# Performance work log

Hardware: AMD Instinct MI355X
Metric: run time of the kernel (lower is better)

Reference implementation:

```python
import jax, jax.numpy as jnp
import numpy as np

N = 120000          # number of edges
DN = 256            # dim_node
DE = 256            # dim_edge
DA = 256            # dim_atten
H = 8               # num_heads
d_n = DN // H       # 32
d_e = DE // H       # 32
d_o = DA // H       # 32
SIGMA = 1.0
SCALE = 0.02


def setup_inputs() -> dict:
    key = jax.random.key(0)
    ks = jax.random.split(key, 16)
    rn = lambda k, s: jax.random.normal(k, s, dtype=jnp.float32)
    HID = DN + 2 * DE  # nn_edge hidden width (bidirectional variant) = 768
    return {
        "query": rn(ks[0], (N, DN)),
        "edge": rn(ks[1], (N, DE)),
        "value": rn(ks[2], (N, DN)),
        "reverse_edge": rn(ks[3], (N, DE)),
        "src_centers": rn(ks[4], (N, 3)),
        "dst_centers": rn(ks[5], (N, 3)),
        # nn_edge: Linear(2*DN+2*DE -> HID) + ReLU, Linear(HID -> DE)
        "We1": rn(ks[6], (2 * DN + 2 * DE, HID)) * SCALE,
        "be1": jnp.zeros((HID,), jnp.float32),
        "We2": rn(ks[7], (HID, DE)) * SCALE,
        "be2": jnp.zeros((DE,), jnp.float32),
        # proj_query / proj_edge / proj_value: single Linear layers
        "Wq": rn(ks[8], (DN, DN)) * SCALE,
        "bq": jnp.zeros((DN,), jnp.float32),
        "Wpe": rn(ks[9], (DE, DE)) * SCALE,
        "bpe": jnp.zeros((DE,), jnp.float32),
        "Wv": rn(ks[10], (DN, DA)) * SCALE,
        "bv": jnp.zeros((DA,), jnp.float32),
        # attention nn (MLP of 1x1 convs over channel dim): (d_n+d_e)->(d_n+d_e)->d_o
        "A1": rn(ks[11], (d_n + d_e, d_n + d_e)) * SCALE,
        "a1": jnp.zeros((d_n + d_e,), jnp.float32),
        "A2": rn(ks[12], (d_n + d_e, d_o)) * SCALE,
        "a2": jnp.zeros((d_o,), jnp.float32),
    }


def reference(query, edge, value, reverse_edge, src_centers, dst_centers,
              We1, be1, We2, be2, Wq, bq, Wpe, bpe, Wv, bv, A1, a1, A2, a2):
    # --- edge feature MLP (bidirectional) ---
    ef_in = jnp.concatenate([query, edge, reverse_edge, value], axis=1)  # [N, 1024]
    h = jax.nn.relu(ef_in @ We1 + be1)
    edge_feature = h @ We2 + be2                                         # [N, DE]

    # --- gaussian distance weights from object centers ---
    dist = jnp.linalg.norm(src_centers - dst_centers, axis=1, keepdims=True)  # [N, 1]
    dw = jnp.exp(-dist ** 2 / (2.0 * SIGMA ** 2))                             # [N, 1]
    edge_feature = edge_feature * dw

    # --- multi-head 'fat' attention ---
    value_proj = value @ Wv + bv                                  # [N, DA]
    q = (query @ Wq + bq).reshape(N, d_n, H)                      # [N, d_n, H]
    e = (edge @ Wpe + bpe).reshape(N, d_e, H)                     # [N, d_e, H]
    x_in = jnp.concatenate([q, e], axis=1)                        # [N, d_n+d_e, H]
    # MLP over channel dim (1x1 conv equivalents), ReLU on hidden only
    h2 = jax.nn.relu(jnp.einsum('nch,co->noh', x_in, A1) + a1[None, :, None])
    logits = jnp.einsum('nch,co->noh', h2, A2) + a2[None, :, None]  # [N, d_o, H]
    prob = jax.nn.softmax(logits, axis=1)

    # distance-reweighted attention, renormalized over channel dim
    combined = prob * dw[:, :, None]                               # [N, d_o, H]
    combined = combined / (combined.sum(axis=1, keepdims=True) + 1e-10)
    weights_avg = combined.mean(axis=2)                            # [N, d_o]
    # sum_d weights_avg[n,d] * value_proj[n,a]  ==  weights_avg.sum(1) * value_proj
    # (avoids materializing the [N, d_o, DA] broadcast the torch code creates)
    x = weights_avg.sum(axis=1, keepdims=True) * value_proj        # [N, DA]
    return (x, edge_feature, prob)
```

## Files before the change

### kernel.cpp

```cpp
#include <hip/hip_runtime.h>
#include <stdint.h>

typedef float  f32x4 __attribute__((ext_vector_type(4)));
typedef _Float16 f16x8 __attribute__((ext_vector_type(8)));
typedef _Float16 f16x4 __attribute__((ext_vector_type(4)));

#define OFF_We1T 0
#define OFF_We2T 786432
#define OFF_WqT  983040
#define OFF_WpeT 1048576
#define OFF_WvT  1114112
#define OFF_A1T  1179648
#define OFF_A2T  1183744
#define NHALF    1185792

__device__ __forceinline__ void gl_lds16(const void* g, void* l) {
  __builtin_amdgcn_global_load_lds((const __attribute__((address_space(1))) uint32_t*)g,
                                   (__attribute__((address_space(3))) uint32_t*)l, 16, 0, 0);
}

__device__ __forceinline__ int bake(int k, int n) {
  return (k & ~63) | ((((k >> 3) ^ n) & 7) << 3) | (k & 7);
}

__global__ __launch_bounds__(256) void prep_weights(
    const float* We1, const float* We2, const float* Wq, const float* Wpe,
    const float* Wv, const float* A1, const float* A2,
    const float* bq, const float* bpe,
    _Float16* wsh, float* bqp, float* bpep) {
  int i = blockIdx.x * 256 + threadIdx.x;
  if (i < OFF_We2T) {
    int n = i >> 10, k = i & 1023;
    wsh[i] = (_Float16)We1[bake(k, n) * 768 + n];
  } else if (i < OFF_WqT) {
    int j = i - OFF_We2T; int n = j / 768, k = j - n * 768;
    wsh[i] = (_Float16)We2[bake(k, n) * 256 + n];
  } else if (i < OFF_WpeT) {
    int j = i - OFF_WqT; int n = j >> 8, k = j & 255;
    int sc = ((n & 31) << 3) + (n >> 5);
    wsh[i] = (_Float16)Wq[bake(k, n) * 256 + sc];
  } else if (i < OFF_WvT) {
    int j = i - OFF_WpeT; int n = j >> 8, k = j & 255;
    int sc = ((n & 31) << 3) + (n >> 5);
    wsh[i] = (_Float16)Wpe[bake(k, n) * 256 + sc];
  } else if (i < OFF_A1T) {
    int j = i - OFF_WvT; int n = j >> 8, k = j & 255;
    wsh[i] = (_Float16)Wv[bake(k, n) * 256 + n];
  } else if (i < OFF_A2T) {
    int j = i - OFF_A1T; int o = j >> 6, c = j & 63;
    wsh[i] = (_Float16)A1[bake(c, o) * 64 + o];
  } else if (i < NHALF) {
    int j = i - OFF_A2T; int o = j >> 6, c = j & 63;
    wsh[i] = (_Float16)A2[bake(c, o) * 32 + o];
  } else if (i < NHALF + 256) {
    int j = i - NHALF;
    bqp[j] = bq[((j & 31) << 3) + (j >> 5)];
  } else if (i < NHALF + 512) {
    int j = i - NHALF - 256;
    bpep[j] = bpe[((j & 31) << 3) + (j >> 5)];
  }
}

__global__ __launch_bounds__(256) void prep_dw(const float* s, const float* d,
                                               float* dw, float* fw, int N) {
  int n = blockIdx.x * 256 + threadIdx.x;
  if (n >= N) return;
  float dx = s[3*n] - d[3*n], dy = s[3*n+1] - d[3*n+1], dz = s[3*n+2] - d[3*n+2];
  float d2 = dx*dx + dy*dy + dz*dz;
  float w = expf(-0.5f * d2);
  dw[n] = w;
  fw[n] = w / (w + 1e-10f);
}

struct GP {
  const float* q; const float* e; const float* v; const float* rev;
  const _Float16* wsh;
  const float* be1; const float* be2; const float* bv;
  const float* bqp; const float* bpep;
  const float* dw; const float* fw;
  float* outb;
  int N; int SPLIT;
};

template <int MODE>
__global__ __launch_bounds__(256) void gemm_k(GP p) {
  __shared__ __align__(16) _Float16 smh[4][8192];
  __shared__ float biasL[128];
  __shared__ float scaleL[128];
  const int t = threadIdx.x;
  const int w = t >> 6, lane = t & 63, lr = lane & 15, lk = lane >> 4;
  const int NBX = (MODE == 1) ? 2 : 6;
  const int flat = blockIdx.y * NBX + blockIdx.x;
  const int xcd = flat & 7, kk2 = flat >> 3;
  const int CH = gridDim.y >> 3;
  const int nb = kk2 % NBX;
  const int mb = xcd * CH + kk2 / NBX;
  const int N = p.N, SPLIT = p.SPLIT;
  const int MT = (N + 127) >> 7;
  if (mb >= MT) return;
  const int wrow = (w >> 1) * 64, wcol = (w & 1) * 64;
  float* Xf  = p.outb;
  float* EFf = p.outb + (size_t)N * 256;
  float* PRf = p.outb + (size_t)N * 512;
  _Float16* hp1 = (_Float16*)Xf;
  _Float16* hp2 = (_Float16*)PRf;

  int K, KT; size_t boff; int g = 0, nbl = nb;
  if (MODE == 0)      { K = 1024; KT = 16; boff = (size_t)nb * 128 * 1024; }
  else if (MODE == 1) { K = 768;  KT = 12; boff = OFF_We2T + (size_t)nb * 128 * 768; }
  else { K = 256; KT = 4; g = nb >> 1; nbl = nb & 1;
         size_t wb = (g == 0) ? (size_t)OFF_WqT : (g == 1) ? (size_t)OFF_WpeT : (size_t)OFF_WvT;
         boff = wb + (size_t)nbl * 128 * 256; }
  const _Float16* Bt = p.wsh + boff;

  if (t < 128) {
    int gr = mb * 128 + t; if (gr > N - 1) gr = N - 1;
    if (MODE == 0) biasL[t] = p.be1[nb * 128 + t];
    else if (MODE == 1) { biasL[t] = p.be2[nb * 128 + t]; scaleL[t] = p.dw[gr]; }
    else {
      if (g == 0)      biasL[t] = p.bqp[nbl * 128 + t];
      else if (g == 1) biasL[t] = p.bpep[nbl * 128 + t];
      else { biasL[t] = p.bv[nbl * 128 + t]; scaleL[t] = p.fw[gr]; }
    }
  }

  auto stageB = [&](int kt, int buf) {
#pragma unroll
    for (int i = 0; i < 4; ++i)
      gl_lds16(Bt + (size_t)(i * 32 + (t >> 3)) * K + kt * 64 + (t & 7) * 8,
               (char*)smh[2 + buf] + i * 4096 + w * 1024);
  };
  auto stageA_dma = [&](int kt, int buf) {
    const _Float16* hr = (mb * 128 < SPLIT)
        ? hp1 + (size_t)mb * 128 * 768
        : hp2 + (size_t)(mb * 128 - SPLIT) * 768;
    int rmax = N - 1 - mb * 128;
#pragma unroll
    for (int i = 0; i < 4; ++i) {
      int rl = i * 32 + (t >> 3); if (rl > rmax) rl = rmax;
      gl_lds16(hr + (size_t)rl * 768 + kt * 64 + (t & 7) * 8,
               (char*)smh[buf] + i * 4096 + w * 1024);
    }
  };
  auto loadA = [&](int kt, float4* pre) {
    const float* As; int cc0;
    if (MODE == 0) {
      int gg = kt >> 2;
      As = (gg == 0) ? p.q : (gg == 1) ? p.e : (gg == 2) ? p.rev : p.v;
      cc0 = (kt & 3) * 64;
    } else {
      As = (g == 0) ? p.q : (g == 1) ? p.e : p.v; cc0 = kt * 64;
    }
#pragma unroll
    for (int i = 0; i < 8; ++i) {
      int id = i * 256 + t, row = id >> 4, c4 = id & 15;
      int gr = mb * 128 + row; if (gr > N - 1) gr = N - 1;
      pre[i] = *(const float4*)(As + (size_t)gr * 256 + cc0 + c4 * 4);
    }
  };
  auto writeA = [&](const float4* pre, int buf) {
#pragma unroll
    for (int i = 0; i < 8; ++i) {
      int id = i * 256 + t, row = id >> 4, c4 = id & 15;
      f16x4 hv; hv.x = (_Float16)pre[i].x; hv.y = (_Float16)pre[i].y;
      hv.z = (_Float16)pre[i].z; hv.w = (_Float16)pre[i].w;
      int off = row * 64 + (((((c4 >> 1) ^ row) & 7) << 3) | ((c4 & 1) << 2));
      *(f16x4*)(&smh[buf][off]) = hv;
    }
  };

  f32x4 acc[4][4] = {};
  float4 pre[8];
  if (MODE == 1) stageA_dma(0, 0);
  stageB(0, 0);
  if (MODE != 1) { loadA(0, pre); writeA(pre, 0); }

  for (int kt = 0; kt < KT; ++kt) {
    const int cur = kt & 1;
    __syncthreads();
    const bool more = (kt + 1 < KT);
    if (more) {
      if (MODE == 1) stageA_dma(kt + 1, cur ^ 1);
      else loadA(kt + 1, pre);
      stageB(kt + 1, cur ^ 1);
    }
    const _Float16* Ab = smh[cur];
    const _Float16* Bb = smh[2 + cur];
#pragma unroll
    for (int ks = 0; ks < 2; ++ks) {
      f16x8 af[4], bf[4];
#pragma unroll
      for (int i = 0; i < 4; ++i)
        af[i] = *(const f16x8*)(Ab + (wrow + i * 16 + lr) * 64 + (((ks * 4 + lk) ^ (lr & 7)) << 3));
#pragma unroll
      for (int j = 0; j < 4; ++j)
        bf[j] = *(const f16x8*)(Bb + (wcol + j * 16 + lr) * 64 + (((ks * 4 + lk) ^ (lr & 7)) << 3));
#pragma unroll
      for (int i = 0; i < 4; ++i)
#pragma unroll
        for (int j = 0; j < 4; ++j)
          acc[i][j] = __builtin_amdgcn_mfma_f32_16x16x32_f16(af[i], bf[j], acc[i][j], 0, 0, 0);
    }
    if (more && MODE != 1) writeA(pre, cur ^ 1);
  }
  __syncthreads();

  const bool f16out = (MODE == 0) || (MODE == 2 && g < 2);
  if (f16out) {
    _Float16* Cl = (_Float16*)smh;
#pragma unroll
    for (int i = 0; i < 4; ++i)
#pragma unroll
      for (int j = 0; j < 4; ++j)
#pragma unroll
        for (int ii = 0; ii < 4; ++ii) {
          int r = wrow + i * 16 + lk * 4 + ii, c = wcol + j * 16 + lr;
          float val = acc[i][j][ii] + biasL[c];
          if (MODE == 0) val = fmaxf(val, 0.f);
          Cl[r * 136 + c] = (_Float16)val;
        }
    __syncthreads();
#pragma unroll
    for (int i = 0; i < 8; ++i) {
      int id = i * 256 + t, row = id >> 4, ch = id & 15;
      int gr = mb * 128 + row;
      if (gr < N) {
        f16x8 val = *(const f16x8*)(Cl + row * 136 + ch * 8);
        if (MODE == 0) {
          _Float16* hrow = (gr < SPLIT) ? hp1 + (size_t)gr * 768
                                        : hp2 + (size_t)(gr - SPLIT) * 768;
          int b64 = nb * 128 + ((ch >> 3) << 6);
          *(f16x8*)(hrow + b64 + (((ch ^ gr) & 7) << 3)) = val;
        } else {
          int j0 = nbl * 128 + ch * 8;
          int q = j0 >> 5;
          int G = ((j0 >> 3) & 3) | ((g == 1) ? 4 : 0);
          *(f16x8*)(hp2 + ((size_t)gr * 8 + q) * 64 + (((G ^ q) & 7) << 3)) = val;
        }
      }
    }
  } else {
    float* Cf = (float*)smh;
#pragma unroll
    for (int pp = 0; pp < 2; ++pp) {
      __syncthreads();
      if ((w >> 1) == pp) {
#pragma unroll
        for (int i = 0; i < 4; ++i)
#pragma unroll
          for (int j = 0; j < 4; ++j)
#pragma unroll
            for (int ii = 0; ii < 4; ++ii) {
              int rl = i * 16 + lk * 4 + ii, c = wcol + j * 16 + lr;
              Cf[rl * 132 + c] = (acc[i][j][ii] + biasL[c]) * scaleL[pp * 64 + rl];
            }
      }
      __syncthreads();
#pragma unroll
      for (int i = 0; i < 8; ++i) {
        int id = i * 256 + t, row = id >> 5, ch = id & 31;
        int gr = mb * 128 + pp * 64 + row;
        if (gr < N) {
          float4 val = *(const float4*)(Cf + row * 132 + ch * 4);
          float* dst = (MODE == 1) ? EFf + (size_t)gr * 256 + nb * 128 + ch * 4
                                   : Xf  + (size_t)gr * 256 + nbl * 128 + ch * 4;
          *(float4*)dst = val;
        }
      }
    }
  }
}

__global__ __launch_bounds__(256) void attn_k(GP p, const float* a1, const float* a2) {
  __shared__ __align__(16) char sm[28928];
  _Float16* xinl = (_Float16*)sm;
  _Float16* A1l  = (_Float16*)(sm + 8192);
  _Float16* A2l  = (_Float16*)(sm + 16384);
  float*    lg   = (float*)(sm + 20480);
  const int t = threadIdx.x;
  const int w = t >> 6, lane = t & 63, lr = lane & 15, lk = lane >> 4;
  const int N = p.N;
  float* PRf = p.outb + (size_t)N * 512;
  const _Float16* xing = (const _Float16*)PRf;
  size_t rowbase = (size_t)blockIdx.x * 64;

#pragma unroll
  for (int i = 0; i < 2; ++i)
    gl_lds16(xing + (rowbase + i * 32 + (t >> 3)) * 64 + (t & 7) * 8,
             sm + i * 4096 + w * 1024);
#pragma unroll
  for (int i = 0; i < 2; ++i)
    gl_lds16(p.wsh + OFF_A1T + (size_t)(i * 32 + (t >> 3)) * 64 + (t & 7) * 8,
             sm + 8192 + i * 4096 + w * 1024);
  gl_lds16(p.wsh + OFF_A2T + (size_t)(t >> 3) * 64 + (t & 7) * 8,
           sm + 16384 + w * 1024);
  __syncthreads();

  f32x4 acc1[4] = {};
#pragma unroll
  for (int ks = 0; ks < 2; ++ks) {
    f16x8 a = *(const f16x8*)(xinl + (w * 16 + lr) * 64 + (((ks * 4 + lk) ^ (lr & 7)) << 3));
#pragma unroll
    for (int j = 0; j < 4; ++j) {
      f16x8 b = *(const f16x8*)(A1l + (j * 16 + lr) * 64 + (((ks * 4 + lk) ^ (lr & 7)) << 3));
      acc1[j] = __builtin_amdgcn_mfma_f32_16x16x32_f16(a, b, acc1[j], 0, 0, 0);
    }
  }
  __syncthreads();
#pragma unroll
  for (int j = 0; j < 4; ++j) {
    float bb = a1[j * 16 + lr];
#pragma unroll
    for (int ii = 0; ii < 4; ++ii) {
      float hv = fmaxf(acc1[j][ii] + bb, 0.f);
      int row2 = w * 16 + lk * 4 + ii, col = j * 16 + lr;
      xinl[row2 * 64 + (((((col >> 3) ^ row2) & 7) << 3) | (col & 7))] = (_Float16)hv;
    }
  }
  __syncthreads();
  f32x4 acc2[2] = {};
#pragma unroll
  for (int ks = 0; ks < 2; ++ks) {
    f16x8 a = *(const f16x8*)(xinl + (w * 16 + lr) * 64 + (((ks * 4 + lk) ^ (lr & 7)) << 3));
#pragma unroll
    for (int j = 0; j < 2; ++j) {
      f16x8 b = *(const f16x8*)(A2l + (j * 16 + lr) * 64 + (((ks * 4 + lk) ^ (lr & 7)) << 3));
      acc2[j] = __builtin_amdgcn_mfma_f32_16x16x32_f16(a, b, acc2[j], 0, 0, 0);
    }
  }
#pragma unroll
  for (int j = 0; j < 2; ++j) {
    float bb = a2[j * 16 + lr];
#pragma unroll
    for (int ii = 0; ii < 4; ++ii)
      lg[(w * 16 + lk * 4 + ii) * 33 + j * 16 + lr] = acc2[j][ii] + bb;
  }
  __syncthreads();
  {
    int r = t >> 2, pq = t & 3;
    float vv[8];
#pragma unroll
    for (int jj = 0; jj < 8; ++jj) vv[jj] = lg[r * 33 + pq * 8 + jj];
    float mx = vv[0];
#pragma unroll
    for (int jj = 1; jj < 8; ++jj) mx = fmaxf(mx, vv[jj]);
    mx = fmaxf(mx, __shfl_xor(mx, 1));
    mx = fmaxf(mx, __shfl_xor(mx, 2));
    float s = 0.f;
#pragma unroll
    for (int jj = 0; jj < 8; ++jj) { vv[jj] = __expf(vv[jj] - mx); s += vv[jj]; }
    s += __shfl_xor(s, 1);
    s += __shfl_xor(s, 2);
    float inv = 1.f / s;
#pragma unroll
    for (int jj = 0; jj < 8; ++jj) lg[r * 33 + pq * 8 + jj] = vv[jj] * inv;
  }
  __syncthreads();
#pragma unroll
  for (int i = 0; i < 8; ++i) {
    int id = i * 256 + t; int hh = id & 7, o = (id >> 3) & 31, nl = id >> 8;
    PRf[(rowbase / 8 + nl) * 256 + o * 8 + hh] = lg[(nl * 8 + hh) * 33 + o];
  }
}

extern "C" void kernel_launch(void* const* d_in, const int* in_sizes, int n_in,
                              void* d_out, int out_size, void* d_ws, size_t ws_size,
                              hipStream_t stream) {
  const float* query = (const float*)d_in[0];
  const float* edge  = (const float*)d_in[1];
  const float* value = (const float*)d_in[2];
  const float* rev   = (const float*)d_in[3];
  const float* srcc  = (const float*)d_in[4];
  const float* dstc  = (const float*)d_in[5];
  const float* We1 = (const float*)d_in[6];  const float* be1 = (const float*)d_in[7];
  const float* We2 = (const float*)d_in[8];  const float* be2 = (const float*)d_in[9];
  const float* Wq  = (const float*)d_in[10]; const float* bq  = (const float*)d_in[11];
  const float* Wpe = (const float*)d_in[12]; const float* bpe = (const float*)d_in[13];
  const float* Wv  = (const float*)d_in[14]; const float* bv  = (const float*)d_in[15];
  const float* A1  = (const float*)d_in[16]; const float* a1  = (const float*)d_in[17];
  const float* A2  = (const float*)d_in[18]; const float* a2  = (const float*)d_in[19];
  const int N = in_sizes[0] / 256;

  _Float16* wsh = (_Float16*)d_ws;
  float* wsf = (float*)d_ws;
  float* dwA  = wsf + NHALF / 2;
  float* fwA  = dwA + N;
  float* bqp  = fwA + N;
  float* bpep = bqp + 256;

  prep_weights<<<(NHALF + 512 + 255) / 256, 256, 0, stream>>>(
      We1, We2, Wq, Wpe, Wv, A1, A2, bq, bpe, wsh, bqp, bpep);
  prep_dw<<<(N + 255) / 256, 256, 0, stream>>>(srcc, dstc, dwA, fwA, N);

  GP p;
  p.q = query; p.e = edge; p.v = value; p.rev = rev;
  p.wsh = wsh; p.be1 = be1; p.be2 = be2; p.bv = bv;
  p.bqp = bqp; p.bpep = bpep; p.dw = dwA; p.fw = fwA;
  p.outb = (float*)d_out; p.N = N; p.SPLIT = (N * 2) / 3;

  const int MT = (N + 127) >> 7;
  const int MTP = (MT + 7) & ~7;
  gemm_k<0><<<dim3(6, MTP), 256, 0, stream>>>(p);
  gemm_k<1><<<dim3(2, MTP), 256, 0, stream>>>(p);
  gemm_k<2><<<dim3(6, MTP), 256, 0, stream>>>(p);
  attn_k<<<N / 8, 256, 0, stream>>>(p, a1, a2);
}
```

Baseline: 1.258 ms.

## Single-buffer GEMM LDS tiles to raise occupancy to four blocks per CU

Replaces the double-buffered A/B shared-memory tiles with one buffer each, cutting LDS use roughly in half, and adds a launch bound of four blocks per multiprocessor. The main loop now computes on the current tile, then synchronizes, stages the next A and B tiles, and synchronizes again. Global loads of A are still prefetched into registers before compute. This trades in-block overlap of DMA staging and MFMA for more resident blocks to hide latency, and it adds a second barrier per K step. The smh array is enlarged to 8704 halves, presumably so the 128x136 epilogue staging buffer still fits.

Result: slower. 1.660 ms (+32.0%).

```diff
diff --git a/kernel.cpp b/kernel.cpp
--- a/kernel.cpp
+++ b/kernel.cpp
@@ -83,8 +83,8 @@
 };
 
 template <int MODE>
-__global__ __launch_bounds__(256) void gemm_k(GP p) {
-  __shared__ __align__(16) _Float16 smh[4][8192];
+__global__ __launch_bounds__(256, 4) void gemm_k(GP p) {
+  __shared__ __align__(16) _Float16 smh[2][8704];
   __shared__ float biasL[128];
   __shared__ float scaleL[128];
   const int t = threadIdx.x;
@@ -124,13 +124,13 @@
     }
   }
 
-  auto stageB = [&](int kt, int buf) {
+  auto stageB = [&](int kt) {
 #pragma unroll
     for (int i = 0; i < 4; ++i)
       gl_lds16(Bt + (size_t)(i * 32 + (t >> 3)) * K + kt * 64 + (t & 7) * 8,
-               (char*)smh[2 + buf] + i * 4096 + w * 1024);
+               (char*)smh[1] + i * 4096 + w * 1024);
   };
-  auto stageA_dma = [&](int kt, int buf) {
+  auto stageA_dma = [&](int kt) {
     const _Float16* hr = (mb * 128 < SPLIT)
         ? hp1 + (size_t)mb * 128 * 768
         : hp2 + (size_t)(mb * 128 - SPLIT) * 768;
@@ -139,7 +139,7 @@
     for (int i = 0; i < 4; ++i) {
       int rl = i * 32 + (t >> 3); if (rl > rmax) rl = rmax;
       gl_lds16(hr + (size_t)rl * 768 + kt * 64 + (t & 7) * 8,
-               (char*)smh[buf] + i * 4096 + w * 1024);
+               (char*)smh[0] + i * 4096 + w * 1024);
     }
   };
   auto loadA = [&](int kt, float4* pre) {
@@ -158,50 +158,49 @@
       pre[i] = *(const float4*)(As + (size_t)gr * 256 + cc0 + c4 * 4);
     }
   };
-  auto writeA = [&](const float4* pre, int buf) {
+  auto writeA = [&](const float4* pre) {
 #pragma unroll
     for (int i = 0; i < 8; ++i) {
       int id = i * 256 + t, row = id >> 4, c4 = id & 15;
       f16x4 hv; hv.x = (_Float16)pre[i].x; hv.y = (_Float16)pre[i].y;
       hv.z = (_Float16)pre[i].z; hv.w = (_Float16)pre[i].w;
       int off = row * 64 + (((((c4 >> 1) ^ row) & 7) << 3) | ((c4 & 1) << 2));
-      *(f16x4*)(&smh[buf][off]) = hv;
+      *(f16x4*)(&smh[0][off]) = hv;
     }
   };
 
   f32x4 acc[4][4] = {};
   float4 pre[8];
-  if (MODE == 1) stageA_dma(0, 0);
-  stageB(0, 0);
-  if (MODE != 1) { loadA(0, pre); writeA(pre, 0); }
+  if (MODE == 1) stageA_dma(0);
+  else { loadA(0, pre); writeA(pre); }
+  stageB(0);
+  __syncthreads();
 
   for (int kt = 0; kt < KT; ++kt) {
-    const int cur = kt & 1;
-    __syncthreads();
     const bool more = (kt + 1 < KT);
-    if (more) {
-      if (MODE == 1) stageA_dma(kt + 1, cur ^ 1);
-      else loadA(kt + 1, pre);
-      stageB(kt + 1, cur ^ 1);
-    }
-    const _Float16* Ab = smh[cur];
-    const _Float16* Bb = smh[2 + cur];
+    if (more && MODE != 1) loadA(kt + 1, pre);
 #pragma unroll
     for (int ks = 0; ks < 2; ++ks) {
       f16x8 af[4], bf[4];
 #pragma unroll
       for (int i = 0; i < 4; ++i)
-        af[i] = *(const f16x8*)(Ab + (wrow + i * 16 + lr) * 64 + (((ks * 4 + lk) ^ (lr & 7)) << 3));
+        af[i] = *(const f16x8*)(smh[0] + (wrow + i * 16 + lr) * 64 + (((ks * 4 + lk) ^ (lr & 7)) << 3));
 #pragma unroll
       for (int j = 0; j < 4; ++j)
-        bf[j] = *(const f16x8*)(Bb + (wcol + j * 16 + lr) * 64 + (((ks * 4 + lk) ^ (lr & 7)) << 3));
+        bf[j] = *(const f16x8*)(smh[1] + (wcol + j * 16 + lr) * 64 + (((ks * 4 + lk) ^ (lr & 7)) << 3));
 #pragma unroll
       for (int i = 0; i < 4; ++i)
 #pragma unroll
         for (int j = 0; j < 4; ++j)
           acc[i][j] = __builtin_amdgcn_mfma_f32_16x16x32_f16(af[i], bf[j], acc[i][j], 0, 0, 0);
     }
-    if (more && MODE != 1) writeA(pre, cur ^ 1);
+    if (more) {
+      __syncthreads();
+      if (MODE == 1) stageA_dma(kt + 1);
+      else writeA(pre);
+      stageB(kt + 1);
+      __syncthreads();
+    }
   }
   __syncthreads();
 
```
